# Kernel optimization log

Hardware: AMD Instinct MI355X
Metric: run time of the kernel (lower is better)

Reference implementation:

```python
import jax, jax.numpy as jnp
import numpy as np

EMBED = 1024
HEADS = 16
HEAD_DIM = EMBED // HEADS


def setup_inputs() -> dict:
    key = jax.random.key(0)
    ks = jax.random.split(key, 9)
    N, L = 2, 2048
    values = jax.random.normal(ks[0], (N, L, EMBED), dtype=jnp.float32)
    keys = jax.random.normal(ks[1], (N, L, EMBED), dtype=jnp.float32)
    query = jax.random.normal(ks[2], (N, L, EMBED), dtype=jnp.float32)
    mask = jax.random.randint(ks[3], (N, 1, L, L), 0, 2, dtype=jnp.int32)
    s = 1.0 / np.sqrt(HEAD_DIM)
    Wv = jax.random.normal(ks[4], (HEAD_DIM, HEAD_DIM), dtype=jnp.float32) * s
    Wk = jax.random.normal(ks[5], (HEAD_DIM, HEAD_DIM), dtype=jnp.float32) * s
    Wq = jax.random.normal(ks[6], (HEAD_DIM, HEAD_DIM), dtype=jnp.float32) * s
    Wout = jax.random.normal(ks[7], (EMBED, EMBED), dtype=jnp.float32) * (1.0 / np.sqrt(EMBED))
    bout = jax.random.normal(ks[8], (EMBED,), dtype=jnp.float32) * 0.01
    return {"values": values, "keys": keys, "query": query, "mask": mask,
            "Wv": Wv, "Wk": Wk, "Wq": Wq, "Wout": Wout, "bout": bout}


def reference(values, keys, query, mask, Wv, Wk, Wq, Wout, bout):
    N, Lq, _ = query.shape
    Lk = keys.shape[1]
    # split heads: [N, L, H, D]
    v = values.reshape(N, Lk, HEADS, HEAD_DIM)
    k = keys.reshape(N, Lk, HEADS, HEAD_DIM)
    q = query.reshape(N, Lq, HEADS, HEAD_DIM)
    # per-head Linear (weight shared across heads), torch Linear: x @ W.T
    v = jnp.einsum('nlhd,ed->nlhe', v, Wv)
    k = jnp.einsum('nlhd,ed->nlhe', k, Wk)
    q = jnp.einsum('nlhd,ed->nlhe', q, Wq)
    # scores [N, H, Q, K]
    scores = jnp.einsum('nqhd,nkhd->nhqk', q, k)
    scores = jnp.where(mask == 0, jnp.float32(-1e20), scores)
    # NOTE: original scales by sqrt(embed_size), not sqrt(head_dim)
    attn = jax.nn.softmax(scores / jnp.sqrt(jnp.float32(EMBED)), axis=3)
    out = jnp.einsum('nhqk,nkhd->nqhd', attn, v).reshape(N, Lq, EMBED)
    return out @ Wout.T + bout
```

## Files before the change

### kernel.cpp

```cpp
#include <hip/hip_runtime.h>
#include <hip/hip_bf16.h>
#include <stdint.h>

typedef unsigned short u16;
typedef __attribute__((ext_vector_type(8))) short short8;
typedef __attribute__((ext_vector_type(4))) float float4_;

#define N_B   2
#define L_SEQ 2048
#define H_N   16
#define D_H   64
#define EMB   1024
#define KWORDS (L_SEQ/64)

#define C2 0.045084220027780106f

#define KP_OFF 0u
#define VP_OFF (8u*1024u*1024u)
#define X2_OFF (16u*1024u*1024u)
#define MP_OFF (24u*1024u*1024u)
#define WB_OFF (25u*1024u*1024u)

__device__ __forceinline__ u16 f2bf(float f) {
    __hip_bfloat16 h = __float2bfloat16(f);
    return *reinterpret_cast<u16*>(&h);
}
__device__ __forceinline__ short8 load8f(const float* p) {
    float4_ a = *(const float4_*)p;
    float4_ b = *(const float4_*)(p + 4);
    short8 r;
    r[0] = (short)f2bf(a[0]); r[1] = (short)f2bf(a[1]);
    r[2] = (short)f2bf(a[2]); r[3] = (short)f2bf(a[3]);
    r[4] = (short)f2bf(b[0]); r[5] = (short)f2bf(b[1]);
    r[6] = (short)f2bf(b[2]); r[7] = (short)f2bf(b[3]);
    return r;
}
__device__ __forceinline__ void gload16(const void* g, void* l) {
    __builtin_amdgcn_global_load_lds(
        (const __attribute__((address_space(1))) uint32_t*)(size_t)g,
        (__attribute__((address_space(3))) uint32_t*)(size_t)l, 16, 0, 0);
}

__global__ __launch_bounds__(256) void maskpack_kernel(const int* __restrict__ mask,
                                                       unsigned long long* __restrict__ mp) {
    int wid  = (blockIdx.x * 256 + threadIdx.x) >> 6;
    int lane = threadIdx.x & 63;
    int m = mask[(size_t)wid * 64 + lane];
    unsigned long long bits = __ballot(m != 0);
    if (lane == 0) mp[wid] = bits;
}

__global__ __launch_bounds__(256) void cvtw_kernel(const float* __restrict__ in,
                                                   u16* __restrict__ o) {
    int i = (blockIdx.x * 256 + threadIdx.x) * 8;
    short8 v = load8f(in + i);
    *(short8*)(o + i) = v;
}

__global__ __launch_bounds__(256) void proj_kernel(const float* __restrict__ x,
                                                   const float* __restrict__ W,
                                                   u16* __restrict__ o) {
    int bid = blockIdx.x;
    int lt = bid & 31;
    int h  = (bid >> 5) & 15;
    int n  = bid >> 9;
    int tid = threadIdx.x;
    int w = tid >> 6, lane = tid & 63;
    int g = lane >> 4, r16 = lane & 15;
    int l0 = lt * 64 + w * 16;

    const float* xrow = x + ((size_t)(n * L_SEQ + l0 + r16)) * EMB + h * 64;
    short8 a0 = load8f(xrow + 8 * g);
    short8 a1 = load8f(xrow + 32 + 8 * g);

    short8 wb[4][2];
    for (int eb = 0; eb < 4; eb++)
        for (int ch = 0; ch < 2; ch++)
            wb[eb][ch] = load8f(W + (eb * 16 + r16) * 64 + ch * 32 + 8 * g);

    float4_ acc[4];
    for (int eb = 0; eb < 4; eb++) {
        float4_ c = {0.f, 0.f, 0.f, 0.f};
        c = __builtin_amdgcn_mfma_f32_16x16x32_bf16(a0, wb[eb][0], c, 0, 0, 0);
        c = __builtin_amdgcn_mfma_f32_16x16x32_bf16(a1, wb[eb][1], c, 0, 0, 0);
        acc[eb] = c;
    }

    u16* ob = o + ((size_t)((n * H_N + h) * L_SEQ + l0)) * 64;
    for (int eb = 0; eb < 4; eb++)
        for (int i = 0; i < 4; i++) {
            int row = 4 * g + i;
            ob[(size_t)row * 64 + eb * 16 + r16] = f2bf(acc[eb][i]);
        }
}

__global__ __launch_bounds__(256) void projt_kernel(const float* __restrict__ x,
                                                    const float* __restrict__ W,
                                                    u16* __restrict__ o) {
    int bid = blockIdx.x;
    int lt = bid & 31;
    int h  = (bid >> 5) & 15;
    int n  = bid >> 9;
    int tid = threadIdx.x;
    int w = tid >> 6, lane = tid & 63;
    int g = lane >> 4, r16 = lane & 15;
    int l0 = lt * 64 + w * 16;

    const float* xrow = x + ((size_t)(n * L_SEQ + l0 + r16)) * EMB + h * 64;
    short8 a0 = load8f(xrow + 8 * g);
    short8 a1 = load8f(xrow + 32 + 8 * g);

    short8 wb[4][2];
    for (int eb = 0; eb < 4; eb++)
        for (int ch = 0; ch < 2; ch++)
            wb[eb][ch] = load8f(W + (eb * 16 + r16) * 64 + ch * 32 + 8 * g);

    float4_ acc[4];
    for (int eb = 0; eb < 4; eb++) {
        float4_ c = {0.f, 0.f, 0.f, 0.f};
        c = __builtin_amdgcn_mfma_f32_16x16x32_bf16(wb[eb][0], a0, c, 0, 0, 0);
        c = __builtin_amdgcn_mfma_f32_16x16x32_bf16(wb[eb][1], a1, c, 0, 0, 0);
        acc[eb] = c;
    }

    u16* obase = o + ((size_t)(n * H_N + h)) * (64 * L_SEQ) + l0 + r16;
    for (int eb = 0; eb < 4; eb++)
        for (int i = 0; i < 4; i++)
            obase[(size_t)(eb * 16 + 4 * g + i) * L_SEQ] = f2bf(acc[eb][i]);
}

__global__ __launch_bounds__(256) void attn_kernel(const float* __restrict__ query,
                                                   const float* __restrict__ Wq,
                                                   const u16* __restrict__ kp,
                                                   const u16* __restrict__ vpT,
                                                   const unsigned long long* __restrict__ mp,
                                                   u16* __restrict__ x2) {
    __shared__ __align__(16) u16 Ks[64 * 64];
    __shared__ __align__(16) u16 Vt[64 * 64];
    __shared__ __align__(16) u16 Pt[4][16 * 64];

    int bid = blockIdx.x;
    int nh = bid & 31, qt = bid >> 5;
    int n = nh >> 4;
    int h = nh & 15;
    int tid = threadIdx.x;
    int w = tid >> 6, lane = tid & 63;
    int g = lane >> 4, r16 = lane & 15;
    int q0 = qt * 64 + w * 16;

    const u16* kb  = kp  + ((size_t)nh * L_SEQ) * 64;
    const u16* vtb = vpT + ((size_t)nh) * (64 * L_SEQ);

    {
        const float* qrow = query + ((size_t)(n * L_SEQ + q0 + r16)) * EMB + h * 64;
        short8 a0 = load8f(qrow + 8 * g);
        short8 a1 = load8f(qrow + 32 + 8 * g);
        for (int eb = 0; eb < 4; eb++) {
            short8 w0 = load8f(Wq + (eb * 16 + r16) * 64 + 8 * g);
            short8 w1 = load8f(Wq + (eb * 16 + r16) * 64 + 32 + 8 * g);
            float4_ c = {0.f, 0.f, 0.f, 0.f};
            c = __builtin_amdgcn_mfma_f32_16x16x32_bf16(a0, w0, c, 0, 0, 0);
            c = __builtin_amdgcn_mfma_f32_16x16x32_bf16(a1, w1, c, 0, 0, 0);
            for (int i = 0; i < 4; i++) {
                int row = 4 * g + i;
                int col = eb * 16 + r16;
                *(u16*)((char*)Pt[w] + row * 128 + ((col * 2) ^ ((row & 7) << 4))) = f2bf(c[i] * C2);
            }
        }
    }
    short8 aq0 = *(const short8*)((char*)Pt[w] + r16 * 128 + ((16 * g) ^ ((r16 & 7) << 4)));
    short8 aq1 = *(const short8*)((char*)Pt[w] + r16 * 128 + ((64 + 16 * g) ^ ((r16 & 7) << 4)));

    float4_ o[4] = {};
    float lpart = 0.f;
    const unsigned long long* mprow = mp + ((size_t)n * L_SEQ + q0 + r16) * KWORDS;

    int rs = (w << 3) + (lane >> 3);
    int cc = (lane & 7) ^ ((lane >> 3) & 7);
    char* ldsK0 = (char*)Ks + w * 1024;
    char* ldsV0 = (char*)Vt + w * 1024;

    for (int kt = 0; kt < 32; kt++) {
        int k0 = kt * 64;
        __syncthreads();
        for (int h2 = 0; h2 < 2; h2++) {
            int r = rs + 32 * h2;
            gload16(kb  + (size_t)(k0 + r) * 64 + cc * 8, ldsK0 + h2 * 4096);
            gload16(vtb + (size_t)r * L_SEQ + k0 + cc * 8, ldsV0 + h2 * 4096);
        }
        __syncthreads();

        unsigned long long word = mprow[kt];

        for (int cb = 0; cb < 4; cb++) {
            int row = cb * 16 + r16;
            int sw = (row & 7) << 4;
            short8 bk0 = *(const short8*)((char*)Ks + row * 128 + ((16 * g) ^ sw));
            short8 bk1 = *(const short8*)((char*)Ks + row * 128 + ((64 + 16 * g) ^ sw));
            float4_ c = {0.f, 0.f, 0.f, 0.f};
            c = __builtin_amdgcn_mfma_f32_16x16x32_bf16(bk0, aq0, c, 0, 0, 0);
            c = __builtin_amdgcn_mfma_f32_16x16x32_bf16(bk1, aq1, c, 0, 0, 0);

            uint32_t wb4 = (uint32_t)((word >> (16 * cb + 4 * g)) & 0xFull);
            float p0 = (wb4 & 1u) ? exp2f(c[0]) : 0.f;
            float p1 = (wb4 & 2u) ? exp2f(c[1]) : 0.f;
            float p2 = (wb4 & 4u) ? exp2f(c[2]) : 0.f;
            float p3 = (wb4 & 8u) ? exp2f(c[3]) : 0.f;
            lpart += (p0 + p1) + (p2 + p3);
            uint32_t lo = (uint32_t)f2bf(p0) | ((uint32_t)f2bf(p1) << 16);
            uint32_t hi = (uint32_t)f2bf(p2) | ((uint32_t)f2bf(p3) << 16);
            uint2 pkv; pkv.x = lo; pkv.y = hi;
            *(uint2*)((char*)Pt[w] + r16 * 128 + (((cb * 32 + 8 * g)) ^ ((r16 & 7) << 4))) = pkv;
        }

        short8 pb0 = *(const short8*)((char*)Pt[w] + r16 * 128 + ((16 * g) ^ ((r16 & 7) << 4)));
        short8 pb1 = *(const short8*)((char*)Pt[w] + r16 * 128 + ((64 + 16 * g) ^ ((r16 & 7) << 4)));

        for (int db = 0; db < 4; db++) {
            int row = db * 16 + r16;
            int sw = (row & 7) << 4;
            short8 av0 = *(const short8*)((char*)Vt + row * 128 + ((16 * g) ^ sw));
            short8 av1 = *(const short8*)((char*)Vt + row * 128 + ((64 + 16 * g) ^ sw));
            o[db] = __builtin_amdgcn_mfma_f32_16x16x32_bf16(av0, pb0, o[db], 0, 0, 0);
            o[db] = __builtin_amdgcn_mfma_f32_16x16x32_bf16(av1, pb1, o[db], 0, 0, 0);
        }
    }

    float tot = lpart;
    tot += __shfl_xor(tot, 16);
    tot += __shfl_xor(tot, 32);
    float inv = 1.f / fmaxf(tot, 1e-30f);

    u16* ob = x2 + ((size_t)(n * L_SEQ + q0 + r16)) * EMB + h * 64;
    for (int db = 0; db < 4; db++)
        for (int i = 0; i < 4; i++)
            ob[db * 16 + 4 * g + i] = f2bf(o[db][i] * inv);
}

__global__ __launch_bounds__(512) void outgemm_kernel(const u16* __restrict__ x2,
                                                      const u16* __restrict__ Wb,
                                                      const float* __restrict__ bout,
                                                      float* __restrict__ out) {
    __shared__ __align__(16) u16 As[128 * 64];
    __shared__ __align__(16) u16 Bs[128 * 64];

    int bid = blockIdx.x;
    int mt = bid >> 3, nt = bid & 7;
    int m0 = mt * 128, n0 = nt * 128;
    int tid = threadIdx.x;
    int w = tid >> 6, lane = tid & 63;
    int g = lane >> 4, r16 = lane & 15;
    int wr = w >> 2, wc = w & 3;

    float4_ acc[4][2] = {};

    int srow = tid >> 2;
    int sq   = tid & 3;

    for (int kbk = 0; kbk < 16; kbk++) {
        int kk0 = kbk * 64;
        __syncthreads();
        for (int j = 0; j < 2; j++) {
            short8 av = *(const short8*)(x2 + (size_t)(m0 + srow) * EMB + kk0 + sq * 16 + j * 8);
            *(short8*)((char*)As + srow * 128 + ((sq * 32 + j * 16) ^ ((srow & 7) << 4))) = av;
            short8 bv = *(const short8*)(Wb + (size_t)(n0 + srow) * EMB + kk0 + sq * 16 + j * 8);
            *(short8*)((char*)Bs + srow * 128 + ((sq * 32 + j * 16) ^ ((srow & 7) << 4))) = bv;
        }
        __syncthreads();

        short8 afr[4][2], bfr[2][2];
        for (int sm = 0; sm < 4; sm++)
            for (int ch = 0; ch < 2; ch++) {
                int row = wr * 64 + sm * 16 + r16;
                afr[sm][ch] = *(const short8*)((char*)As + row * 128 + ((ch * 64 + 16 * g) ^ ((row & 7) << 4)));
            }
        for (int sn = 0; sn < 2; sn++)
            for (int ch = 0; ch < 2; ch++) {
                int row = wc * 32 + sn * 16 + r16;
                bfr[sn][ch] = *(const short8*)((char*)Bs + row * 128 + ((ch * 64 + 16 * g) ^ ((row & 7) << 4)));
            }
        for (int sm = 0; sm < 4; sm++)
            for (int sn = 0; sn < 2; sn++) {
                acc[sm][sn] = __builtin_amdgcn_mfma_f32_16x16x32_bf16(afr[sm][0], bfr[sn][0], acc[sm][sn], 0, 0, 0);
                acc[sm][sn] = __builtin_amdgcn_mfma_f32_16x16x32_bf16(afr[sm][1], bfr[sn][1], acc[sm][sn], 0, 0, 0);
            }
    }

    for (int sm = 0; sm < 4; sm++)
        for (int sn = 0; sn < 2; sn++) {
            int nn = n0 + wc * 32 + sn * 16 + r16;
            float bv = bout[nn];
            for (int i = 0; i < 4; i++) {
                int mm = m0 + wr * 64 + sm * 16 + 4 * g + i;
                out[(size_t)mm * EMB + nn] = acc[sm][sn][i] + bv;
            }
        }
}

extern "C" void kernel_launch(void* const* d_in, const int* in_sizes, int n_in,
                              void* d_out, int out_size, void* d_ws, size_t ws_size,
                              hipStream_t stream) {
    const float* values = (const float*)d_in[0];
    const float* keys   = (const float*)d_in[1];
    const float* query  = (const float*)d_in[2];
    const int*   mask   = (const int*)d_in[3];
    const float* Wv     = (const float*)d_in[4];
    const float* Wk     = (const float*)d_in[5];
    const float* Wq     = (const float*)d_in[6];
    const float* Wout   = (const float*)d_in[7];
    const float* bout   = (const float*)d_in[8];
    float* out = (float*)d_out;

    char* ws = (char*)d_ws;
    u16* kp  = (u16*)(ws + KP_OFF);
    u16* vpT = (u16*)(ws + VP_OFF);
    u16* x2  = (u16*)(ws + X2_OFF);
    unsigned long long* mpk = (unsigned long long*)(ws + MP_OFF);
    u16* wb  = (u16*)(ws + WB_OFF);

    maskpack_kernel<<<32768, 256, 0, stream>>>(mask, mpk);
    cvtw_kernel<<<512, 256, 0, stream>>>(Wout, wb);
    proj_kernel<<<1024, 256, 0, stream>>>(keys, Wk, kp);
    projt_kernel<<<1024, 256, 0, stream>>>(values, Wv, vpT);
    attn_kernel<<<1024, 256, 0, stream>>>(query, Wq, kp, vpT, mpk, x2);
    outgemm_kernel<<<256, 512, 0, stream>>>(x2, wb, bout, out);
}
```

Baseline: 260.6 us.

## Merge prep kernels, double attention query tile, use async LDS loads in out GEMM

```diff
diff --git a/kernel.cpp b/kernel.cpp
--- a/kernel.cpp
+++ b/kernel.cpp
@@ -20,6 +20,11 @@
 #define X2_OFF (16u*1024u*1024u)
 #define MP_OFF (24u*1024u*1024u)
 #define WB_OFF (25u*1024u*1024u)
+
+#define PREP_MASK  32768u
+#define PREP_CVTW  (PREP_MASK + 512u)
+#define PREP_PROJK (PREP_CVTW + 1024u)
+#define PREP_TOTAL (PREP_PROJK + 1024u)
 
 __device__ __forceinline__ u16 f2bf(float f) {
     __hip_bfloat16 h = __float2bfloat16(f);
@@ -40,31 +45,47 @@
         (const __attribute__((address_space(1))) uint32_t*)(size_t)g,
         (__attribute__((address_space(3))) uint32_t*)(size_t)l, 16, 0, 0);
 }
-
-__global__ __launch_bounds__(256) void maskpack_kernel(const int* __restrict__ mask,
-                                                       unsigned long long* __restrict__ mp) {
-    int wid  = (blockIdx.x * 256 + threadIdx.x) >> 6;
-    int lane = threadIdx.x & 63;
-    int m = mask[(size_t)wid * 64 + lane];
-    unsigned long long bits = __ballot(m != 0);
-    if (lane == 0) mp[wid] = bits;
-}
-
-__global__ __launch_bounds__(256) void cvtw_kernel(const float* __restrict__ in,
-                                                   u16* __restrict__ o) {
-    int i = (blockIdx.x * 256 + threadIdx.x) * 8;
-    short8 v = load8f(in + i);
-    *(short8*)(o + i) = v;
-}
-
-__global__ __launch_bounds__(256) void proj_kernel(const float* __restrict__ x,
-                                                   const float* __restrict__ W,
-                                                   u16* __restrict__ o) {
-    int bid = blockIdx.x;
-    int lt = bid & 31;
-    int h  = (bid >> 5) & 15;
-    int n  = bid >> 9;
+__device__ __forceinline__ uint32_t cvtpk(float a, float b) {
+    uint32_t r;
+    asm("v_cvt_pk_bf16_f32 %0, %1, %2" : "=v"(r) : "v"(a), "v"(b));
+    return r;
+}
+
+__global__ __launch_bounds__(256) void prep_kernel(const int* __restrict__ mask,
+                                                   unsigned long long* __restrict__ mp,
+                                                   const float* __restrict__ Wout,
+                                                   u16* __restrict__ wb,
+                                                   const float* __restrict__ keys,
+                                                   const float* __restrict__ Wk,
+                                                   u16* __restrict__ kp,
+                                                   const float* __restrict__ values,
+                                                   const float* __restrict__ Wv,
+                                                   u16* __restrict__ vpT) {
+    unsigned bid = blockIdx.x;
     int tid = threadIdx.x;
+
+    if (bid < PREP_MASK) {
+        int wid  = (bid * 256 + tid) >> 6;
+        int lane = tid & 63;
+        int m = mask[(size_t)wid * 64 + lane];
+        unsigned long long bits = __ballot(m != 0);
+        if (lane == 0) mp[wid] = bits;
+        return;
+    }
+    if (bid < PREP_CVTW) {
+        int i = ((bid - PREP_MASK) * 256 + tid) * 8;
+        *(short8*)(wb + i) = load8f(Wout + i);
+        return;
+    }
+
+    bool isK = bid < PREP_PROJK;
+    unsigned lb = bid - (isK ? PREP_CVTW : PREP_PROJK);
+    const float* x = isK ? keys : values;
+    const float* W = isK ? Wk : Wv;
+
+    int lt = lb & 31;
+    int h  = (lb >> 5) & 15;
+    int n  = lb >> 9;
     int w = tid >> 6, lane = tid & 63;
     int g = lane >> 4, r16 = lane & 15;
     int l0 = lt * 64 + w * 16;
@@ -73,60 +94,30 @@
     short8 a0 = load8f(xrow + 8 * g);
     short8 a1 = load8f(xrow + 32 + 8 * g);
 
-    short8 wb[4][2];
+    short8 wf[4][2];
     for (int eb = 0; eb < 4; eb++)
         for (int ch = 0; ch < 2; ch++)
-            wb[eb][ch] = load8f(W + (eb * 16 + r16) * 64 + ch * 32 + 8 * g);
-
-    float4_ acc[4];
-    for (int eb = 0; eb < 4; eb++) {
-        float4_ c = {0.f, 0.f, 0.f, 0.f};
-        c = __builtin_amdgcn_mfma_f32_16x16x32_bf16(a0, wb[eb][0], c, 0, 0, 0);
-        c = __builtin_amdgcn_mfma_f32_16x16x32_bf16(a1, wb[eb][1], c, 0, 0, 0);
-        acc[eb] = c;
-    }
-
-    u16* ob = o + ((size_t)((n * H_N + h) * L_SEQ + l0)) * 64;
-    for (int eb = 0; eb < 4; eb++)
-        for (int i = 0; i < 4; i++) {
-            int row = 4 * g + i;
-            ob[(size_t)row * 64 + eb * 16 + r16] = f2bf(acc[eb][i]);
-        }
-}
-
-__global__ __launch_bounds__(256) void projt_kernel(const float* __restrict__ x,
-                                                    const float* __restrict__ W,
-                                                    u16* __restrict__ o) {
-    int bid = blockIdx.x;
-    int lt = bid & 31;
-    int h  = (bid >> 5) & 15;
-    int n  = bid >> 9;
-    int tid = threadIdx.x;
-    int w = tid >> 6, lane = tid & 63;
-    int g = lane >> 4, r16 = lane & 15;
-    int l0 = lt * 64 + w * 16;
-
-    const float* xrow = x + ((size_t)(n * L_SEQ + l0 + r16)) * EMB + h * 64;
-    short8 a0 = load8f(xrow + 8 * g);
-    short8 a1 = load8f(xrow + 32 + 8 * g);
-
-    short8 wb[4][2];
-    for (int eb = 0; eb < 4; eb++)
-        for (int ch = 0; ch < 2; ch++)
-            wb[eb][ch] = load8f(W + (eb * 16 + r16) * 64 + ch * 32 + 8 * g);
-
-    float4_ acc[4];
-    for (int eb = 0; eb < 4; eb++) {
-        float4_ c = {0.f, 0.f, 0.f, 0.f};
-        c = __builtin_amdgcn_mfma_f32_16x16x32_bf16(wb[eb][0], a0, c, 0, 0, 0);
-        c = __builtin_amdgcn_mfma_f32_16x16x32_bf16(wb[eb][1], a1, c, 0, 0, 0);
-        acc[eb] = c;
-    }
-
-    u16* obase = o + ((size_t)(n * H_N + h)) * (64 * L_SEQ) + l0 + r16;
-    for (int eb = 0; eb < 4; eb++)
-        for (int i = 0; i < 4; i++)
-            obase[(size_t)(eb * 16 + 4 * g + i) * L_SEQ] = f2bf(acc[eb][i]);
+            wf[eb][ch] = load8f(W + (eb * 16 + r16) * 64 + ch * 32 + 8 * g);
+
+    if (isK) {
+        u16* ob = kp + ((size_t)((n * H_N + h) * L_SEQ + l0)) * 64;
+        for (int eb = 0; eb < 4; eb++) {
+            float4_ c = {0.f, 0.f, 0.f, 0.f};
+            c = __builtin_amdgcn_mfma_f32_16x16x32_bf16(a0, wf[eb][0], c, 0, 0, 0);
+            c = __builtin_amdgcn_mfma_f32_16x16x32_bf16(a1, wf[eb][1], c, 0, 0, 0);
+            for (int i = 0; i < 4; i++)
+                ob[(size_t)(4 * g + i) * 64 + eb * 16 + r16] = f2bf(c[i]);
+        }
+    } else {
+        u16* obase = vpT + ((size_t)(n * H_N + h)) * (64 * L_SEQ) + l0 + r16;
+        for (int eb = 0; eb < 4; eb++) {
+            float4_ c = {0.f, 0.f, 0.f, 0.f};
+            c = __builtin_amdgcn_mfma_f32_16x16x32_bf16(wf[eb][0], a0, c, 0, 0, 0);
+            c = __builtin_amdgcn_mfma_f32_16x16x32_bf16(wf[eb][1], a1, c, 0, 0, 0);
+            for (int i = 0; i < 4; i++)
+                obase[(size_t)(eb * 16 + 4 * g + i) * L_SEQ] = f2bf(c[i]);
+        }
+    }
 }
 
 __global__ __launch_bounds__(256) void attn_kernel(const float* __restrict__ query,
@@ -137,7 +128,7 @@
                                                    u16* __restrict__ x2) {
     __shared__ __align__(16) u16 Ks[64 * 64];
     __shared__ __align__(16) u16 Vt[64 * 64];
-    __shared__ __align__(16) u16 Pt[4][16 * 64];
+    __shared__ __align__(16) u16 Pt[4][2][16 * 64];
 
     int bid = blockIdx.x;
     int nh = bid & 31, qt = bid >> 5;
@@ -146,34 +137,41 @@
     int tid = threadIdx.x;
     int w = tid >> 6, lane = tid & 63;
     int g = lane >> 4, r16 = lane & 15;
-    int q0 = qt * 64 + w * 16;
+    int q0 = qt * 128 + w * 16;
 
     const u16* kb  = kp  + ((size_t)nh * L_SEQ) * 64;
     const u16* vtb = vpT + ((size_t)nh) * (64 * L_SEQ);
 
-    {
-        const float* qrow = query + ((size_t)(n * L_SEQ + q0 + r16)) * EMB + h * 64;
+    int psw = (r16 & 7) << 4;
+
+    short8 wf[4][2];
+    for (int eb = 0; eb < 4; eb++)
+        for (int ch = 0; ch < 2; ch++)
+            wf[eb][ch] = load8f(Wq + (eb * 16 + r16) * 64 + ch * 32 + 8 * g);
+
+    for (int s = 0; s < 2; s++) {
+        const float* qrow = query + ((size_t)(n * L_SEQ + q0 + s * 64 + r16)) * EMB + h * 64;
         short8 a0 = load8f(qrow + 8 * g);
         short8 a1 = load8f(qrow + 32 + 8 * g);
         for (int eb = 0; eb < 4; eb++) {
-            short8 w0 = load8f(Wq + (eb * 16 + r16) * 64 + 8 * g);
-            short8 w1 = load8f(Wq + (eb * 16 + r16) * 64 + 32 + 8 * g);
             float4_ c = {0.f, 0.f, 0.f, 0.f};
-            c = __builtin_amdgcn_mfma_f32_16x16x32_bf16(a0, w0, c, 0, 0, 0);
-            c = __builtin_amdgcn_mfma_f32_16x16x32_bf16(a1, w1, c, 0, 0, 0);
+            c = __builtin_amdgcn_mfma_f32_16x16x32_bf16(a0, wf[eb][0], c, 0, 0, 0);
+            c = __builtin_amdgcn_mfma_f32_16x16x32_bf16(a1, wf[eb][1], c, 0, 0, 0);
             for (int i = 0; i < 4; i++) {
                 int row = 4 * g + i;
-                int col = eb * 16 + r16;
-                *(u16*)((char*)Pt[w] + row * 128 + ((col * 2) ^ ((row & 7) << 4))) = f2bf(c[i] * C2);
-            }
-        }
-    }
-    short8 aq0 = *(const short8*)((char*)Pt[w] + r16 * 128 + ((16 * g) ^ ((r16 & 7) << 4)));
-    short8 aq1 = *(const short8*)((char*)Pt[w] + r16 * 128 + ((64 + 16 * g) ^ ((r16 & 7) << 4)));
-
-    float4_ o[4] = {};
-    float lpart = 0.f;
-    const unsigned long long* mprow = mp + ((size_t)n * L_SEQ + q0 + r16) * KWORDS;
+                *(u16*)((char*)Pt[w][s] + row * 128 + (((eb * 16 + r16) * 2) ^ ((row & 7) << 4))) = f2bf(c[i] * C2);
+            }
+        }
+    }
+    short8 aq00 = *(const short8*)((char*)Pt[w][0] + r16 * 128 + ((16 * g) ^ psw));
+    short8 aq01 = *(const short8*)((char*)Pt[w][0] + r16 * 128 + ((64 + 16 * g) ^ psw));
+    short8 aq10 = *(const short8*)((char*)Pt[w][1] + r16 * 128 + ((16 * g) ^ psw));
+    short8 aq11 = *(const short8*)((char*)Pt[w][1] + r16 * 128 + ((64 + 16 * g) ^ psw));
+
+    float4_ o0[4] = {}, o1[4] = {};
+    float lp0 = 0.f, lp1 = 0.f;
+    const unsigned long long* mprow0 = mp + ((size_t)n * L_SEQ + q0 + r16) * KWORDS;
+    const unsigned long long* mprow1 = mprow0 + (size_t)64 * KWORDS;
 
     int rs = (w << 3) + (lane >> 3);
     int cc = (lane & 7) ^ ((lane >> 3) & 7);
@@ -190,51 +188,74 @@
         }
         __syncthreads();
 
-        unsigned long long word = mprow[kt];
+        unsigned long long word0 = mprow0[kt];
+        unsigned long long word1 = mprow1[kt];
 
         for (int cb = 0; cb < 4; cb++) {
             int row = cb * 16 + r16;
             int sw = (row & 7) << 4;
             short8 bk0 = *(const short8*)((char*)Ks + row * 128 + ((16 * g) ^ sw));
             short8 bk1 = *(const short8*)((char*)Ks + row * 128 + ((64 + 16 * g) ^ sw));
-            float4_ c = {0.f, 0.f, 0.f, 0.f};
-            c = __builtin_amdgcn_mfma_f32_16x16x32_bf16(bk0, aq0, c, 0, 0, 0);
-            c = __builtin_amdgcn_mfma_f32_16x16x32_bf16(bk1, aq1, c, 0, 0, 0);
-
-            uint32_t wb4 = (uint32_t)((word >> (16 * cb + 4 * g)) & 0xFull);
-            float p0 = (wb4 & 1u) ? exp2f(c[0]) : 0.f;
-            float p1 = (wb4 & 2u) ? exp2f(c[1]) : 0.f;
-            float p2 = (wb4 & 4u) ? exp2f(c[2]) : 0.f;
-            float p3 = (wb4 & 8u) ? exp2f(c[3]) : 0.f;
-            lpart += (p0 + p1) + (p2 + p3);
-            uint32_t lo = (uint32_t)f2bf(p0) | ((uint32_t)f2bf(p1) << 16);
-            uint32_t hi = (uint32_t)f2bf(p2) | ((uint32_t)f2bf(p3) << 16);
-            uint2 pkv; pkv.x = lo; pkv.y = hi;
-            *(uint2*)((char*)Pt[w] + r16 * 128 + (((cb * 32 + 8 * g)) ^ ((r16 & 7) << 4))) = pkv;
-        }
-
-        short8 pb0 = *(const short8*)((char*)Pt[w] + r16 * 128 + ((16 * g) ^ ((r16 & 7) << 4)));
-        short8 pb1 = *(const short8*)((char*)Pt[w] + r16 * 128 + ((64 + 16 * g) ^ ((r16 & 7) << 4)));
+            float4_ c0 = {0.f, 0.f, 0.f, 0.f};
+            c0 = __builtin_amdgcn_mfma_f32_16x16x32_bf16(bk0, aq00, c0, 0, 0, 0);
+            c0 = __builtin_amdgcn_mfma_f32_16x16x32_bf16(bk1, aq01, c0, 0, 0, 0);
+            float4_ c1 = {0.f, 0.f, 0.f, 0.f};
+            c1 = __builtin_amdgcn_mfma_f32_16x16x32_bf16(bk0, aq10, c1, 0, 0, 0);
+            c1 = __builtin_amdgcn_mfma_f32_16x16x32_bf16(bk1, aq11, c1, 0, 0, 0);
+
+            uint32_t nib0 = (uint32_t)(word0 >> (16 * cb + 4 * g)) & 0xFu;
+            uint32_t nib1 = (uint32_t)(word1 >> (16 * cb + 4 * g)) & 0xFu;
+
+            float p0 = (nib0 & 1u) ? exp2f(c0[0]) : 0.f;
+            float p1 = (nib0 & 2u) ? exp2f(c0[1]) : 0.f;
+            float p2 = (nib0 & 4u) ? exp2f(c0[2]) : 0.f;
+            float p3 = (nib0 & 8u) ? exp2f(c0[3]) : 0.f;
+            lp0 += (p0 + p1) + (p2 + p3);
+            uint2 pk0; pk0.x = cvtpk(p0, p1); pk0.y = cvtpk(p2, p3);
+            *(uint2*)((char*)Pt[w][0] + r16 * 128 + ((cb * 32 + 8 * g) ^ psw)) = pk0;
+
+            float q0v = (nib1 & 1u) ? exp2f(c1[0]) : 0.f;
+            float q1v = (nib1 & 2u) ? exp2f(c1[1]) : 0.f;
+            float q2v = (nib1 & 4u) ? exp2f(c1[2]) : 0.f;
+            float q3v = (nib1 & 8u) ? exp2f(c1[3]) : 0.f;
+            lp1 += (q0v + q1v) + (q2v + q3v);
+            uint2 pk1; pk1.x = cvtpk(q0v, q1v); pk1.y = cvtpk(q2v, q3v);
+            *(uint2*)((char*)Pt[w][1] + r16 * 128 + ((cb * 32 + 8 * g) ^ psw)) = pk1;
+        }
+
+        short8 pb00 = *(const short8*)((char*)Pt[w][0] + r16 * 128 + ((16 * g) ^ psw));
+        short8 pb01 = *(const short8*)((char*)Pt[w][0] + r16 * 128 + ((64 + 16 * g) ^ psw));
+        short8 pb10 = *(const short8*)((char*)Pt[w][1] + r16 * 128 + ((16 * g) ^ psw));
+        short8 pb11 = *(const short8*)((char*)Pt[w][1] + r16 * 128 + ((64 + 16 * g) ^ psw));
 
         for (int db = 0; db < 4; db++) {
             int row = db * 16 + r16;
             int sw = (row & 7) << 4;
             short8 av0 = *(const short8*)((char*)Vt + row * 128 + ((16 * g) ^ sw));
             short8 av1 = *(const short8*)((char*)Vt + row * 128 + ((64 + 16 * g) ^ sw));
-            o[db] = __builtin_amdgcn_mfma_f32_16x16x32_bf16(av0, pb0, o[db], 0, 0, 0);
-            o[db] = __builtin_amdgcn_mfma_f32_16x16x32_bf16(av1, pb1, o[db], 0, 0, 0);
-        }
-    }
-
-    float tot = lpart;
-    tot += __shfl_xor(tot, 16);
-    tot += __shfl_xor(tot, 32);
-    float inv = 1.f / fmaxf(tot, 1e-30f);
-
-    u16* ob = x2 + ((size_t)(n * L_SEQ + q0 + r16)) * EMB + h * 64;
+            o0[db] = __builtin_amdgcn_mfma_f32_16x16x32_bf16(av0, pb00, o0[db], 0, 0, 0);
+            o0[db] = __builtin_amdgcn_mfma_f32_16x16x32_bf16(av1, pb01, o0[db], 0, 0, 0);
+            o1[db] = __builtin_amdgcn_mfma_f32_16x16x32_bf16(av0, pb10, o1[db], 0, 0, 0);
+            o1[db] = __builtin_amdgcn_mfma_f32_16x16x32_bf16(av1, pb11, o1[db], 0, 0, 0);
+        }
+    }
+
+    float t0 = lp0;
+    t0 += __shfl_xor(t0, 16);
+    t0 += __shfl_xor(t0, 32);
+    float inv0 = 1.f / fmaxf(t0, 1e-30f);
+    float t1 = lp1;
+    t1 += __shfl_xor(t1, 16);
+    t1 += __shfl_xor(t1, 32);
+    float inv1 = 1.f / fmaxf(t1, 1e-30f);
+
+    u16* ob0 = x2 + ((size_t)(n * L_SEQ + q0 + r16)) * EMB + h * 64;
+    u16* ob1 = x2 + ((size_t)(n * L_SEQ + q0 + 64 + r16)) * EMB + h * 64;
     for (int db = 0; db < 4; db++)
-        for (int i = 0; i < 4; i++)
-            ob[db * 16 + 4 * g + i] = f2bf(o[db][i] * inv);
+        for (int i = 0; i < 4; i++) {
+            ob0[db * 16 + 4 * g + i] = f2bf(o0[db][i] * inv0);
+            ob1[db * 16 + 4 * g + i] = f2bf(o1[db][i] * inv1);
+        }
 }
 
 __global__ __launch_bounds__(512) void outgemm_kernel(const u16* __restrict__ x2,
@@ -254,17 +275,18 @@
 
     float4_ acc[4][2] = {};
 
-    int srow = tid >> 2;
-    int sq   = tid & 3;
+    int rs = (w << 3) + (lane >> 3);
+    int cc = (lane & 7) ^ ((lane >> 3) & 7);
+    char* ldsA0 = (char*)As + w * 1024;
+    char* ldsB0 = (char*)Bs + w * 1024;
 
     for (int kbk = 0; kbk < 16; kbk++) {
         int kk0 = kbk * 64;
         __syncthreads();
-        for (int j = 0; j < 2; j++) {
-            short8 av = *(const short8*)(x2 + (size_t)(m0 + srow) * EMB + kk0 + sq * 16 + j * 8);
-            *(short8*)((char*)As + srow * 128 + ((sq * 32 + j * 16) ^ ((srow & 7) << 4))) = av;
-            short8 bv = *(const short8*)(Wb + (size_t)(n0 + srow) * EMB + kk0 + sq * 16 + j * 8);
-            *(short8*)((char*)Bs + srow * 128 + ((sq * 32 + j * 16) ^ ((srow & 7) << 4))) = bv;
+        for (int h2 = 0; h2 < 2; h2++) {
+            int r = rs + 64 * h2;
+            gload16(x2 + (size_t)(m0 + r) * EMB + kk0 + cc * 8, ldsA0 + h2 * 8192);
+            gload16(Wb + (size_t)(n0 + r) * EMB + kk0 + cc * 8, ldsB0 + h2 * 8192);
         }
         __syncthreads();
 
@@ -318,10 +340,8 @@
     unsigned long long* mpk = (unsigned long long*)(ws + MP_OFF);
     u16* wb  = (u16*)(ws + WB_OFF);
 
-    maskpack_kernel<<<32768, 256, 0, stream>>>(mask, mpk);
-    cvtw_kernel<<<512, 256, 0, stream>>>(Wout, wb);
-    proj_kernel<<<1024, 256, 0, stream>>>(keys, Wk, kp);
-    projt_kernel<<<1024, 256, 0, stream>>>(values, Wv, vpT);
-    attn_kernel<<<1024, 256, 0, stream>>>(query, Wq, kp, vpT, mpk, x2);
+    prep_kernel<<<PREP_TOTAL, 256, 0, stream>>>(mask, mpk, Wout, wb,
+                                                keys, Wk, kp, values, Wv, vpT);
+    attn_kernel<<<512, 256, 0, stream>>>(query, Wq, kp, vpT, mpk, x2);
     outgemm_kernel<<<256, 512, 0, stream>>>(x2, wb, bout, out);
 }
```

Result: faster. 252.4 us (-3.1%).
